# Kernel optimization log

Hardware: AMD Instinct MI355X
Metric: run time of the kernel (lower is better)

Reference implementation:

```python
import jax, jax.numpy as jnp
import numpy as np

TINY = np.finfo(np.float32).tiny


def setup_inputs() -> dict:
    key = jax.random.key(0)
    k1, k2, k3 = jax.random.split(key, 3)
    B, IN, OUT = 4096, 4096, 1024
    x = jax.random.normal(k1, (B, IN), dtype=jnp.float32)
    weight = jax.random.normal(k2, (IN, OUT), dtype=jnp.float32)
    uniform = jax.random.uniform(k3, (IN, OUT), dtype=jnp.float32)
    T = jnp.ones((1,), dtype=jnp.float32)
    return {"x": x, "weight": weight, "uniform": uniform, "T": T}


def reference(x, weight, uniform, T):
    # training-path forward of ConcreteLayer
    # uniform -> (1 - tiny) * u + tiny, then Gumbel noise
    u = (1.0 - TINY) * uniform + TINY
    gumbel = -jnp.log(-jnp.log(u))                      # [in, out]
    noisy_logits = (weight + gumbel) / T                # temperature scaling
    samples = jax.nn.softmax(noisy_logits, axis=1)      # softmax over out dim (torch default for 2D)
    out = jnp.einsum('bi,ik->bk', x, samples)           # [batch, out]
    return out
```

## Files before the change

### kernel.cpp

```cpp
#include <hip/hip_runtime.h>
#include <cstdint>
#include <cstddef>


#define TINYF 1.17549435082228750797e-38f
#define LN2F 0.69314718055994530942f
#define LOG2EF 1.44269504088896340736f

typedef unsigned short u16;
typedef __attribute__((ext_vector_type(8))) short bf16x8;
typedef __attribute__((ext_vector_type(4))) float f32x4;

__device__ __forceinline__ u16 f2bf(float f) {
  union { float f; uint32_t u; } v; v.f = f;
  uint32_t r = v.u + 0x7FFFu + ((v.u >> 16) & 1u);
  return (u16)(r >> 16);
}
__device__ __forceinline__ float bf2f(u16 h) {
  union { float f; uint32_t u; } v; v.u = ((uint32_t)h) << 16;
  return v.f;
}

__device__ __forceinline__ float log2_hw(float x) { return __builtin_amdgcn_logf(x); }
__device__ __forceinline__ float exp2_hw(float x) { return __builtin_amdgcn_exp2f(x); }

__device__ __forceinline__ float gumbel_fast(float u) {
  float t = -log2_hw(u);
  return -LN2F * log2_hw(t * LN2F);
}
__device__ __forceinline__ float exp_fast(float x) { return exp2_hw(x * LOG2EF); }

__device__ __forceinline__ void gld_lds16(const void* g, void* l) {
  __builtin_amdgcn_global_load_lds(
      (__attribute__((address_space(1))) void*)(g),
      (__attribute__((address_space(3))) void*)(l), 16, 0, 0);
}

#define NB_TRANS 1024
#define NB_CAST 16384
#define NB_ZERO 4096

__global__ void prep_kernel(const float* __restrict__ W, const float* __restrict__ U,
                            const float* __restrict__ Tp, const float4* __restrict__ x,
                            u16* __restrict__ BT, float* __restrict__ dpart,
                            ushort4* __restrict__ xb, float4* __restrict__ out) {
  __shared__ float tile[64][65];
  const int bx = blockIdx.x;
  const int t = threadIdx.x;

  if (bx < NB_TRANS) {
    const int k0 = (bx & 63) * 64, n0 = (bx >> 6) * 64;
    const float invT = 1.0f / Tp[0];
    {
      const int nn4 = (t & 15) * 4, kq = t >> 4;
#pragma unroll
      for (int r = 0; r < 4; ++r) {
        int kk = r * 16 + kq;
        size_t gi = (size_t)(k0 + kk) * 1024 + (n0 + nn4);
        float4 w = *(const float4*)&W[gi];
        float4 u = *(const float4*)&U[gi];
        float e0 = exp_fast((w.x + gumbel_fast(u.x * (1.0f - TINYF) + TINYF)) * invT);
        float e1 = exp_fast((w.y + gumbel_fast(u.y * (1.0f - TINYF) + TINYF)) * invT);
        float e2 = exp_fast((w.z + gumbel_fast(u.z * (1.0f - TINYF) + TINYF)) * invT);
        float e3 = exp_fast((w.w + gumbel_fast(u.w * (1.0f - TINYF) + TINYF)) * invT);
        tile[kk][nn4 + 0] = e0; tile[kk][nn4 + 1] = e1;
        tile[kk][nn4 + 2] = e2; tile[kk][nn4 + 3] = e3;
        float s = (e0 + e1) + (e2 + e3);
#pragma unroll
        for (int m = 8; m > 0; m >>= 1) s += __shfl_xor(s, m, 16);
        if ((t & 15) == 0) dpart[(bx >> 6) * 4096 + k0 + kk] = s;
      }
    }
    __syncthreads();
    {
      const int kk4 = (t & 15) * 4, nq = t >> 4;
#pragma unroll
      for (int r = 0; r < 4; ++r) {
        int nn = r * 16 + nq;
        ushort4 o;
        o.x = f2bf(tile[kk4 + 0][nn]);
        o.y = f2bf(tile[kk4 + 1][nn]);
        o.z = f2bf(tile[kk4 + 2][nn]);
        o.w = f2bf(tile[kk4 + 3][nn]);
        *(ushort4*)&BT[(size_t)(n0 + nn) * 4096 + (k0 + kk4)] = o;
      }
    }
  } else if (bx < NB_TRANS + NB_CAST) {
    int i = (bx - NB_TRANS) * 256 + t;
    float4 v = x[i];
    ushort4 o;
    o.x = f2bf(v.x); o.y = f2bf(v.y); o.z = f2bf(v.z); o.w = f2bf(v.w);
    xb[i] = o;
  } else {
    int j = (bx - NB_TRANS - NB_CAST) * 256 + t;
    out[j] = make_float4(0.f, 0.f, 0.f, 0.f);
  }
}

__global__ void bt_scale_kernel(u16* __restrict__ BT, const float* __restrict__ dpart) {
  __shared__ float invd[128];
  const int c0 = blockIdx.x * 128;
  const int r0 = blockIdx.y * 128;
  const int t = threadIdx.x;
  if (t < 128) {
    float s = 0.f;
#pragma unroll
    for (int p = 0; p < 16; ++p) s += dpart[p * 4096 + c0 + t];
    invd[t] = 1.0f / s;
  }
  __syncthreads();
  const int cv = (t & 15) * 8, rq = t >> 4;
  const float4 ia = *(const float4*)&invd[cv];
  const float4 ib = *(const float4*)&invd[cv + 4];
#pragma unroll
  for (int pass = 0; pass < 8; ++pass) {
    int row = r0 + pass * 16 + rq;
    size_t gi = (size_t)row * 4096 + c0 + cv;
    ushort4 a = *(ushort4*)&BT[gi];
    ushort4 b = *(ushort4*)&BT[gi + 4];
    ushort4 oa, ob;
    oa.x = f2bf(bf2f(a.x) * ia.x); oa.y = f2bf(bf2f(a.y) * ia.y);
    oa.z = f2bf(bf2f(a.z) * ia.z); oa.w = f2bf(bf2f(a.w) * ia.w);
    ob.x = f2bf(bf2f(b.x) * ib.x); ob.y = f2bf(bf2f(b.y) * ib.y);
    ob.z = f2bf(bf2f(b.z) * ib.z); ob.w = f2bf(bf2f(b.w) * ib.w);
    *(ushort4*)&BT[gi] = oa;
    *(ushort4*)&BT[gi + 4] = ob;
  }
}

#define TM 128
#define TN 128
#define TK 64
#define SPLITK 2

__launch_bounds__(256)
__global__ void gemm_bt_kernel(const u16* __restrict__ A, const u16* __restrict__ BT,
                               float* __restrict__ C, int M, int N, int K) {
  __shared__ u16 As[TM * TK];
  __shared__ u16 Bs[TN * TK];

  const int tid = threadIdx.x;
  const int lane = tid & 63, w = tid >> 6;
  const int wm = w >> 1, wn = w & 1;
  const int m0 = blockIdx.x * TM, n0 = blockIdx.y * TN;
  const int quad = lane >> 4, r16 = lane & 15;
  const int srow = lane >> 3;
  const int sg = (lane & 7) ^ srow;

  const int kz = blockIdx.z;
  const int Kh = K >> 1;
  const u16* Ak = A + (size_t)kz * Kh;
  const u16* Bk = BT + (size_t)kz * Kh;

  f32x4 acc[4][4] = {};

  for (int kt = 0; kt < Kh; kt += TK) {
    __syncthreads();
#pragma unroll
    for (int c = 0; c < 4; ++c) {
      int chunk = w * 4 + c;
      gld_lds16(Ak + (size_t)(m0 + chunk * 8 + srow) * K + kt + sg * 8, (char*)As + chunk * 1024);
      gld_lds16(Bk + (size_t)(n0 + chunk * 8 + srow) * K + kt + sg * 8, (char*)Bs + chunk * 1024);
    }
    __syncthreads();

#pragma unroll
    for (int ss = 0; ss < 2; ++ss) {
      bf16x8 aF[4], bF[4];
#pragma unroll
      for (int mi = 0; mi < 4; ++mi) {
        int row = wm * 64 + mi * 16 + r16;
        aF[mi] = *(const bf16x8*)((const char*)As + row * 128 + (((ss * 4 + quad) ^ (row & 7)) * 16));
      }
#pragma unroll
      for (int ni = 0; ni < 4; ++ni) {
        int row = wn * 64 + ni * 16 + r16;
        bF[ni] = *(const bf16x8*)((const char*)Bs + row * 128 + (((ss * 4 + quad) ^ (row & 7)) * 16));
      }
#pragma unroll
      for (int mi = 0; mi < 4; ++mi)
#pragma unroll
        for (int ni = 0; ni < 4; ++ni)
          acc[mi][ni] = __builtin_amdgcn_mfma_f32_16x16x32_bf16(aF[mi], bF[ni], acc[mi][ni], 0, 0, 0);
    }
  }

#pragma unroll
  for (int mi = 0; mi < 4; ++mi)
#pragma unroll
    for (int ni = 0; ni < 4; ++ni)
#pragma unroll
      for (int r = 0; r < 4; ++r) {
        int row = m0 + wm * 64 + mi * 16 + quad * 4 + r;
        int col = n0 + wn * 64 + ni * 16 + r16;
        atomicAdd(&C[(size_t)row * N + col], acc[mi][ni][r]);
      }
}

extern "C" void kernel_launch(void* const* d_in, const int* in_sizes, int n_in,
                              void* d_out, int out_size, void* d_ws, size_t ws_size,
                              hipStream_t stream) {
  const int M = 4096, K = 4096, N = 1024;
  const float* x = (const float*)d_in[0];
  const float* W = (const float*)d_in[1];
  const float* U = (const float*)d_in[2];
  const float* Tp = (const float*)d_in[3];
  float* out = (float*)d_out;

  char* ws = (char*)d_ws;
  u16* xb = (u16*)ws;
  u16* bt = (u16*)(ws + (size_t)M * K * 2);
  float* dpart = (float*)(ws + (size_t)M * K * 2 + (size_t)N * K * 2);

  prep_kernel<<<dim3(NB_TRANS + NB_CAST + NB_ZERO), 256, 0, stream>>>(
      W, U, Tp, (const float4*)x, bt, dpart, (ushort4*)xb, (float4*)out);
  bt_scale_kernel<<<dim3(32, 8), 256, 0, stream>>>(bt, dpart);
  gemm_bt_kernel<<<dim3(M / TM, N / TN, SPLITK), 256, 0, stream>>>(xb, bt, out, M, N, K);
}
```

Measured before the change: 192.7 us.

## Rewrite GEMM as 256x256 double-buffered pipelined kernel with split-K 4

Replaces the 128x128 single-buffered bf16 GEMM with a 256x256 tile, 512-thread kernel. It double-buffers K tiles in 128KB of dynamic LDS and interleaves staged global-to-LDS loads with MFMA phases, using explicit barriers, waitcnts and setprio. The 4-way split-K with a swizzled 1D grid of 256 blocks is meant to fill the CUs while hiding load latency behind compute. The trade is more fp32 atomic traffic on the output and heavy LDS and register pressure.

```diff
diff --git a/kernel.cpp b/kernel.cpp
--- a/kernel.cpp
+++ b/kernel.cpp
@@ -128,72 +128,116 @@
   }
 }
 
-#define TM 128
-#define TN 128
-#define TK 64
-#define SPLITK 2
-
-__launch_bounds__(256)
+#define NT 16
+#define NIT 8
+#define SPLITK 4
+
+__device__ __forceinline__ void stage_ht(const u16* __restrict__ Ak, const u16* __restrict__ Bk,
+                                         int m0, int n0, char* smem, int tile, int ht,
+                                         int w, int lane) {
+  const u16* src = (ht < 2) ? (Ak + (size_t)(m0 + ht * 128) * 4096)
+                            : (Bk + (size_t)(n0 + (ht - 2) * 128) * 4096);
+  char* dst = smem + (tile & 1) * 65536 + ht * 16384;
+  const int rr = lane >> 3;
+  const int gcol = tile * 64 + (((lane & 7) ^ rr) << 3);
+#pragma unroll
+  for (int c = 0; c < 2; ++c) {
+    const int chunk = w * 2 + c;
+    gld_lds16(src + (size_t)(chunk * 8 + rr) * 4096 + gcol, dst + chunk * 1024);
+  }
+}
+
+__launch_bounds__(512, 2)
 __global__ void gemm_bt_kernel(const u16* __restrict__ A, const u16* __restrict__ BT,
-                               float* __restrict__ C, int M, int N, int K) {
-  __shared__ u16 As[TM * TK];
-  __shared__ u16 Bs[TN * TK];
-
-  const int tid = threadIdx.x;
-  const int lane = tid & 63, w = tid >> 6;
-  const int wm = w >> 1, wn = w & 1;
-  const int m0 = blockIdx.x * TM, n0 = blockIdx.y * TN;
-  const int quad = lane >> 4, r16 = lane & 15;
-  const int srow = lane >> 3;
-  const int sg = (lane & 7) ^ srow;
-
-  const int kz = blockIdx.z;
-  const int Kh = K >> 1;
-  const u16* Ak = A + (size_t)kz * Kh;
-  const u16* Bk = BT + (size_t)kz * Kh;
-
-  f32x4 acc[4][4] = {};
-
-  for (int kt = 0; kt < Kh; kt += TK) {
-    __syncthreads();
-#pragma unroll
-    for (int c = 0; c < 4; ++c) {
-      int chunk = w * 4 + c;
-      gld_lds16(Ak + (size_t)(m0 + chunk * 8 + srow) * K + kt + sg * 8, (char*)As + chunk * 1024);
-      gld_lds16(Bk + (size_t)(n0 + chunk * 8 + srow) * K + kt + sg * 8, (char*)Bs + chunk * 1024);
+                               float* __restrict__ C) {
+  extern __shared__ char smem[];
+  int wg = blockIdx.x;
+  wg = (wg & 7) * 32 + (wg >> 3);
+  const int kz = wg >> 6;
+  const int bx = wg & 15, by = (wg >> 4) & 3;
+  const int m0 = bx * 256, n0 = by * 256;
+  const int tid = threadIdx.x, lane = tid & 63, w = tid >> 6;
+  const int wm = w >> 2, wn = w & 3;
+  const int r16 = lane & 15, quad = lane >> 4, r7 = r16 & 7;
+
+  const u16* Ak = A + (size_t)kz * 1024;
+  const u16* Bk = BT + (size_t)kz * 1024;
+
+  char* abase = smem + wm * 16384 + r16 * 128;
+  char* bbase = smem + 32768 + (wn >> 1) * 16384 + ((wn & 1) * 64 + r16) * 128;
+  const int gx[2] = {(quad ^ r7) * 16, ((4 + quad) ^ r7) * 16};
+
+  bf16x8 aF[4][2], bF[4][2];
+  f32x4 acc[8][4] = {};
+
+#define RD_A(DB, MB)                                                              \
+  _Pragma("unroll") for (int j = 0; j < 4; ++j) {                                 \
+    aF[j][0] = *(const bf16x8*)(abase + (DB) * 65536 + ((MB) + j) * 2048 + gx[0]); \
+    aF[j][1] = *(const bf16x8*)(abase + (DB) * 65536 + ((MB) + j) * 2048 + gx[1]); \
+  }
+#define RD_B(DB, NB)                                                                   \
+  _Pragma("unroll") for (int j = 0; j < 2; ++j) {                                      \
+    bF[(NB) + j][0] = *(const bf16x8*)(bbase + (DB) * 65536 + ((NB) + j) * 2048 + gx[0]); \
+    bF[(NB) + j][1] = *(const bf16x8*)(bbase + (DB) * 65536 + ((NB) + j) * 2048 + gx[1]); \
+  }
+#define MM(MB, NB)                                                                \
+  _Pragma("unroll") for (int mi = 0; mi < 4; ++mi)                                \
+    _Pragma("unroll") for (int nj = 0; nj < 2; ++nj) {                            \
+      acc[(MB) + mi][(NB) + nj] = __builtin_amdgcn_mfma_f32_16x16x32_bf16(        \
+          aF[mi][0], bF[(NB) + nj][0], acc[(MB) + mi][(NB) + nj], 0, 0, 0);       \
+      acc[(MB) + mi][(NB) + nj] = __builtin_amdgcn_mfma_f32_16x16x32_bf16(        \
+          aF[mi][1], bF[(NB) + nj][1], acc[(MB) + mi][(NB) + nj], 0, 0, 0);       \
     }
-    __syncthreads();
-
-#pragma unroll
-    for (int ss = 0; ss < 2; ++ss) {
-      bf16x8 aF[4], bF[4];
-#pragma unroll
-      for (int mi = 0; mi < 4; ++mi) {
-        int row = wm * 64 + mi * 16 + r16;
-        aF[mi] = *(const bf16x8*)((const char*)As + row * 128 + (((ss * 4 + quad) ^ (row & 7)) * 16));
-      }
-#pragma unroll
-      for (int ni = 0; ni < 4; ++ni) {
-        int row = wn * 64 + ni * 16 + r16;
-        bF[ni] = *(const bf16x8*)((const char*)Bs + row * 128 + (((ss * 4 + quad) ^ (row & 7)) * 16));
-      }
-#pragma unroll
-      for (int mi = 0; mi < 4; ++mi)
-#pragma unroll
-        for (int ni = 0; ni < 4; ++ni)
-          acc[mi][ni] = __builtin_amdgcn_mfma_f32_16x16x32_bf16(aF[mi], bF[ni], acc[mi][ni], 0, 0, 0);
-    }
-  }
-
-#pragma unroll
-  for (int mi = 0; mi < 4; ++mi)
+#define PH(READS, STILE, SHT, MFMAS, BOUND)                                       \
+  {                                                                               \
+    READS                                                                         \
+    {                                                                             \
+      int tc = (STILE) < (NT - 1) ? (STILE) : (NT - 1);                           \
+      stage_ht(Ak, Bk, m0, n0, smem, tc, (SHT), w, lane);                         \
+    }                                                                             \
+    __builtin_amdgcn_s_barrier();                                                 \
+    asm volatile("s_waitcnt lgkmcnt(0)" ::: "memory");                            \
+    __builtin_amdgcn_sched_barrier(0);                                            \
+    __builtin_amdgcn_s_setprio(1);                                                \
+    MFMAS                                                                         \
+    __builtin_amdgcn_s_setprio(0);                                                \
+    if (BOUND) asm volatile("s_waitcnt vmcnt(2)" ::: "memory");                   \
+    __builtin_amdgcn_s_barrier();                                                 \
+  }
+
+  stage_ht(Ak, Bk, m0, n0, smem, 0, 0, w, lane);
+  stage_ht(Ak, Bk, m0, n0, smem, 0, 1, w, lane);
+  stage_ht(Ak, Bk, m0, n0, smem, 0, 2, w, lane);
+  stage_ht(Ak, Bk, m0, n0, smem, 0, 3, w, lane);
+  stage_ht(Ak, Bk, m0, n0, smem, 1, 0, w, lane);
+  asm volatile("s_waitcnt vmcnt(2)" ::: "memory");
+  __builtin_amdgcn_s_barrier();
+
+  for (int i = 0; i < NIT; ++i) {
+    const int t1 = 2 * i + 1;
+    PH(RD_A(0, 0) RD_B(0, 0), t1, 1, MM(0, 0), 0)
+    PH(RD_B(0, 2),            t1, 2, MM(0, 2), 0)
+    PH(RD_A(0, 4),            t1, 3, MM(4, 2), 0)
+    PH({},                    t1 + 1, 0, MM(4, 0), 1)
+    PH(RD_A(1, 0) RD_B(1, 0), t1 + 1, 1, MM(0, 0), 0)
+    PH(RD_B(1, 2),            t1 + 1, 2, MM(0, 2), 0)
+    PH(RD_A(1, 4),            t1 + 1, 3, MM(4, 2), 0)
+    PH({},                    t1 + 2, 0, MM(4, 0), 1)
+  }
+#undef RD_A
+#undef RD_B
+#undef MM
+#undef PH
+
+#pragma unroll
+  for (int mi = 0; mi < 8; ++mi)
 #pragma unroll
     for (int ni = 0; ni < 4; ++ni)
 #pragma unroll
       for (int r = 0; r < 4; ++r) {
-        int row = m0 + wm * 64 + mi * 16 + quad * 4 + r;
+        int row = m0 + wm * 128 + mi * 16 + quad * 4 + r;
         int col = n0 + wn * 64 + ni * 16 + r16;
-        atomicAdd(&C[(size_t)row * N + col], acc[mi][ni][r]);
+        atomicAdd(&C[(size_t)row * 1024 + col], acc[mi][ni][r]);
       }
 }
 
@@ -212,8 +256,15 @@
   u16* bt = (u16*)(ws + (size_t)M * K * 2);
   float* dpart = (float*)(ws + (size_t)M * K * 2 + (size_t)N * K * 2);
 
+  static bool attr_done = false;
+  if (!attr_done) {
+    hipFuncSetAttribute((const void*)gemm_bt_kernel,
+                        hipFuncAttributeMaxDynamicSharedMemorySize, 131072);
+    attr_done = true;
+  }
+
   prep_kernel<<<dim3(NB_TRANS + NB_CAST + NB_ZERO), 256, 0, stream>>>(
       W, U, Tp, (const float4*)x, bt, dpart, (ushort4*)xb, (float4*)out);
   bt_scale_kernel<<<dim3(32, 8), 256, 0, stream>>>(bt, dpart);
-  gemm_bt_kernel<<<dim3(M / TM, N / TN, SPLITK), 256, 0, stream>>>(xb, bt, out, M, N, K);
-}
+  gemm_bt_kernel<<<dim3(256), 512, 131072, stream>>>(xb, bt, out);
+}
```

Measured after the change: 224.7 us. +16.6%, slower.

## Load GEMM fragments directly from global into registers with double buffering

Applied to the files above, without the earlier changes.

The GEMM stops staging A and B tiles through LDS with barriers. Each lane now loads its MFMA fragments straight from global memory into registers, with a two-stage register double buffer so the next K-tile loads overlap the current MFMAs. Launch bounds now request two blocks per SM. This removes LDS traffic and syncthreads, but neighbouring waves no longer share loads, so global and L2 traffic rises, and the larger register footprint may limit occupancy.

```diff
diff --git a/kernel.cpp b/kernel.cpp
--- a/kernel.cpp
+++ b/kernel.cpp
@@ -29,12 +29,6 @@
   return -LN2F * log2_hw(t * LN2F);
 }
 __device__ __forceinline__ float exp_fast(float x) { return exp2_hw(x * LOG2EF); }
-
-__device__ __forceinline__ void gld_lds16(const void* g, void* l) {
-  __builtin_amdgcn_global_load_lds(
-      (__attribute__((address_space(1))) void*)(g),
-      (__attribute__((address_space(3))) void*)(l), 16, 0, 0);
-}
 
 #define NB_TRANS 1024
 #define NB_CAST 16384
@@ -130,60 +124,64 @@
 
 #define TM 128
 #define TN 128
-#define TK 64
 #define SPLITK 2
 
-__launch_bounds__(256)
+__launch_bounds__(256, 2)
 __global__ void gemm_bt_kernel(const u16* __restrict__ A, const u16* __restrict__ BT,
                                float* __restrict__ C, int M, int N, int K) {
-  __shared__ u16 As[TM * TK];
-  __shared__ u16 Bs[TN * TK];
-
   const int tid = threadIdx.x;
   const int lane = tid & 63, w = tid >> 6;
   const int wm = w >> 1, wn = w & 1;
   const int m0 = blockIdx.x * TM, n0 = blockIdx.y * TN;
   const int quad = lane >> 4, r16 = lane & 15;
-  const int srow = lane >> 3;
-  const int sg = (lane & 7) ^ srow;
 
   const int kz = blockIdx.z;
   const int Kh = K >> 1;
   const u16* Ak = A + (size_t)kz * Kh;
   const u16* Bk = BT + (size_t)kz * Kh;
 
+  const u16* ap[4];
+  const u16* bp[4];
+#pragma unroll
+  for (int i = 0; i < 4; ++i) {
+    ap[i] = Ak + (size_t)(m0 + wm * 64 + i * 16 + r16) * K + quad * 8;
+    bp[i] = Bk + (size_t)(n0 + wn * 64 + i * 16 + r16) * K + quad * 8;
+  }
+
   f32x4 acc[4][4] = {};
-
-  for (int kt = 0; kt < Kh; kt += TK) {
-    __syncthreads();
-#pragma unroll
-    for (int c = 0; c < 4; ++c) {
-      int chunk = w * 4 + c;
-      gld_lds16(Ak + (size_t)(m0 + chunk * 8 + srow) * K + kt + sg * 8, (char*)As + chunk * 1024);
-      gld_lds16(Bk + (size_t)(n0 + chunk * 8 + srow) * K + kt + sg * 8, (char*)Bs + chunk * 1024);
-    }
-    __syncthreads();
-
-#pragma unroll
-    for (int ss = 0; ss < 2; ++ss) {
-      bf16x8 aF[4], bF[4];
-#pragma unroll
-      for (int mi = 0; mi < 4; ++mi) {
-        int row = wm * 64 + mi * 16 + r16;
-        aF[mi] = *(const bf16x8*)((const char*)As + row * 128 + (((ss * 4 + quad) ^ (row & 7)) * 16));
-      }
-#pragma unroll
-      for (int ni = 0; ni < 4; ++ni) {
-        int row = wn * 64 + ni * 16 + r16;
-        bF[ni] = *(const bf16x8*)((const char*)Bs + row * 128 + (((ss * 4 + quad) ^ (row & 7)) * 16));
-      }
-#pragma unroll
-      for (int mi = 0; mi < 4; ++mi)
-#pragma unroll
-        for (int ni = 0; ni < 4; ++ni)
-          acc[mi][ni] = __builtin_amdgcn_mfma_f32_16x16x32_bf16(aF[mi], bF[ni], acc[mi][ni], 0, 0, 0);
-    }
-  }
+  bf16x8 aF[2][2][4], bF[2][2][4];
+
+#define LDT(BUF, T)                                                                \
+  {                                                                                \
+    _Pragma("unroll") for (int s2 = 0; s2 < 2; ++s2) {                             \
+      _Pragma("unroll") for (int i = 0; i < 4; ++i) {                              \
+        aF[BUF][s2][i] = *(const bf16x8*)(ap[i] + (size_t)(T) * 64 + s2 * 32);     \
+        bF[BUF][s2][i] = *(const bf16x8*)(bp[i] + (size_t)(T) * 64 + s2 * 32);     \
+      }                                                                            \
+    }                                                                              \
+  }
+#define FMT(BUF)                                                                   \
+  {                                                                                \
+    _Pragma("unroll") for (int s2 = 0; s2 < 2; ++s2)                               \
+      _Pragma("unroll") for (int mi = 0; mi < 4; ++mi)                             \
+        _Pragma("unroll") for (int ni = 0; ni < 4; ++ni)                           \
+          acc[mi][ni] = __builtin_amdgcn_mfma_f32_16x16x32_bf16(                   \
+              aF[BUF][s2][mi], bF[BUF][s2][ni], acc[mi][ni], 0, 0, 0);             \
+  }
+
+  const int NTL = Kh / 64;
+  LDT(0, 0)
+  for (int t = 0; t + 2 < NTL; t += 2) {
+    LDT(1, t + 1)
+    FMT(0)
+    LDT(0, t + 2)
+    FMT(1)
+  }
+  LDT(1, NTL - 1)
+  FMT(0)
+  FMT(1)
+#undef LDT
+#undef FMT
 
 #pragma unroll
   for (int mi = 0; mi < 4; ++mi)
```

Result: slower. 260.6 us (+35.2%).
